# Performance work log

Measured on AMD Instinct MI355X. Metric: run time of the kernel, lower is better.

## Reference

```python
import jax, jax.numpy as jnp
import numpy as np

B, N, C, F, P, S = 128, 32, 1024, 14, 3, 2  # batch, boxes/img, channels, fmap size, pooled size, sampling ratio
NUM_BEHAVIORS = 27


def _interp(coords, size):
    # torchvision-style bilinear weights along one axis. coords: [M]
    valid = (coords > -1.0) & (coords < size)
    c = jnp.clip(coords, 0.0, size - 1.0)
    lo = jnp.clip(jnp.floor(c).astype(jnp.int32), 0, size - 2)
    hi = lo + 1
    f = c - lo.astype(c.dtype)
    wlo = jnp.where(valid, 1.0 - f, 0.0)
    whi = jnp.where(valid, f, 0.0)
    return lo, hi, wlo, whi


def _roi_one(fm, box):
    # fm: [C,H,W], box: [4] = (x1,y1,x2,y2) in fmap coords. Returns [C,P,P].
    x1, y1, x2, y2 = box[0], box[1], box[2], box[3]
    roi_w = jnp.maximum(x2 - x1, 1.0)
    roi_h = jnp.maximum(y2 - y1, 1.0)
    bh, bw = roi_h / P, roi_w / P
    offs = (jnp.arange(S, dtype=fm.dtype) + 0.5) / S  # sample offsets within a bin
    bins = jnp.arange(P, dtype=fm.dtype)
    ys = (y1 + bins[:, None] * bh + offs[None, :] * bh).reshape(-1)  # [P*S]
    xs = (x1 + bins[:, None] * bw + offs[None, :] * bw).reshape(-1)  # [P*S]
    ylo, yhi, wylo, wyhi = _interp(ys, F)
    xlo, xhi, wxlo, wxhi = _interp(xs, F)
    # separable bilinear gather: first along H, then along W
    fy = fm[:, ylo, :] * wylo[None, :, None] + fm[:, yhi, :] * wyhi[None, :, None]  # [C,M,W]
    v = fy[:, :, xlo] * wxlo[None, None, :] + fy[:, :, xhi] * wxhi[None, None, :]    # [C,M,M]
    return v.reshape(C, P, S, P, S).mean(axis=(2, 4))


def setup_inputs() -> dict:
    key = jax.random.key(0)
    ks = jax.random.split(key, 9)
    fmap = jax.random.normal(ks[0], (B, C, F, F), dtype=jnp.float32)
    # two random corner candidates per axis -> sorted gives valid (x1,y1,x2,y2) in [0,F]
    raw = jax.random.uniform(ks[1], (B, N, 2, 2), dtype=jnp.float32) * F
    lo = raw.min(axis=2)  # [B,N,2] -> (x1,y1)
    hi = raw.max(axis=2)  # [B,N,2] -> (x2,y2)
    boxes = jnp.concatenate([lo, hi], axis=-1)  # [B,N,4]
    w_c1 = jax.random.normal(ks[2], (512, 1024), dtype=jnp.float32) * 0.03
    w_c2 = jax.random.normal(ks[3], (256, 512), dtype=jnp.float32) * 0.04
    w_fc1 = jax.random.normal(ks[4], (2304, 1024), dtype=jnp.float32) * 0.02
    b_fc1 = jax.random.normal(ks[5], (1024,), dtype=jnp.float32) * 0.01
    w_fc2 = jax.random.normal(ks[6], (1024, NUM_BEHAVIORS), dtype=jnp.float32) * 0.03
    b_fc2 = jax.random.normal(ks[7], (NUM_BEHAVIORS,), dtype=jnp.float32) * 0.01
    return {"fmap": fmap, "boxes": boxes, "w_c1": w_c1, "w_c2": w_c2,
            "w_fc1": w_fc1, "b_fc1": b_fc1, "w_fc2": w_fc2, "b_fc2": b_fc2}


def reference(fmap, boxes, w_c1, w_c2, w_fc1, b_fc1, w_fc2, b_fc2):
    boxes = jnp.clip(boxes, 0.0, float(F))  # torch.clamp(box, 0, fmap_size)
    # per-image, per-box ROIAlign without duplicating fmap per box
    pooled = jax.vmap(lambda fm, bxs: jax.vmap(lambda b: _roi_one(fm, b))(bxs))(fmap, boxes)
    pooled = jax.lax.stop_gradient(pooled)  # fmap.detach() + no_grad roi_align
    x = pooled.reshape(B * N, C, P, P)
    x = jnp.einsum('kchw,oc->kohw', x, w_c1)  # 1x1 conv, no bias
    x = jnp.einsum('kchw,oc->kohw', x, w_c2)  # 1x1 conv, no bias
    x = x.reshape(B * N, -1)                  # [K, 256*3*3] (C,H,W order as in torch .view)
    h = jax.nn.relu(x @ w_fc1 + b_fc1)        # dropout inactive (eval / deterministic ref)
    logits = h @ w_fc2 + b_fc2                # [K, num_behaviors]
    return logits
```

## Files before the change

kernel.cpp:

```cpp
#include <hip/hip_runtime.h>

typedef unsigned short ushortT;
typedef __attribute__((ext_vector_type(8))) short short8;
typedef __attribute__((ext_vector_type(4))) short short4v;
typedef __attribute__((ext_vector_type(8))) __bf16 bf16x8;
typedef __attribute__((ext_vector_type(4))) float f32x4;

__device__ __forceinline__ float bf2f(ushortT u) {
    unsigned int x = ((unsigned int)u) << 16;
    return __builtin_bit_cast(float, x);
}
__device__ __forceinline__ ushortT f2bf(float f) {
    unsigned int x = __builtin_bit_cast(unsigned int, f);
    unsigned int r = (x + 0x7FFFu + ((x >> 16) & 1u)) >> 16;
    return (ushortT)r;
}

__device__ __forceinline__ void gload_lds16(const void* g, void* l) {
    __builtin_amdgcn_global_load_lds(
        (const __attribute__((address_space(1))) void*)g,
        (__attribute__((address_space(3))) void*)l, 16, 0, 0);
}

__global__ __launch_bounds__(256)
void build_wct_part(const float* __restrict__ w_c1, const float* __restrict__ w_c2,
                    float* __restrict__ part)
{
    __shared__ float w2s[64][65];
    __shared__ float w1s[64][65];
    const int o0 = blockIdx.x * 64;
    const int c0 = blockIdx.y * 64;
    const int m0 = blockIdx.z * 128;
    const int tid = threadIdx.x;
    const int ty = tid >> 4, tx = tid & 15;
    float acc[4][4] = {};
    for (int mm = 0; mm < 128; mm += 64) {
        #pragma unroll
        for (int c4 = 0; c4 < 4; ++c4) {
            int idx = c4 * 256 + tid;
            int row = idx >> 4, f4 = idx & 15;
            float4 v = *reinterpret_cast<const float4*>(
                w_c2 + (size_t)(o0 + row) * 512 + m0 + mm + f4 * 4);
            w2s[row][f4*4+0] = v.x; w2s[row][f4*4+1] = v.y;
            w2s[row][f4*4+2] = v.z; w2s[row][f4*4+3] = v.w;
            float4 u = *reinterpret_cast<const float4*>(
                w_c1 + (size_t)(m0 + mm + row) * 1024 + c0 + f4 * 4);
            w1s[row][f4*4+0] = u.x; w1s[row][f4*4+1] = u.y;
            w1s[row][f4*4+2] = u.z; w1s[row][f4*4+3] = u.w;
        }
        __syncthreads();
        for (int m = 0; m < 64; ++m) {
            float a[4], b[4];
            #pragma unroll
            for (int i = 0; i < 4; ++i) a[i] = w2s[ty*4+i][m];
            #pragma unroll
            for (int j = 0; j < 4; ++j) b[j] = w1s[m][tx*4+j];
            #pragma unroll
            for (int i = 0; i < 4; ++i)
                #pragma unroll
                for (int j = 0; j < 4; ++j) acc[i][j] = fmaf(a[i], b[j], acc[i][j]);
        }
        __syncthreads();
    }
    float* dst = part + (size_t)blockIdx.z * 262144;
    #pragma unroll
    for (int i = 0; i < 4; ++i) {
        float4 ov = { acc[i][0], acc[i][1], acc[i][2], acc[i][3] };
        *reinterpret_cast<float4*>(dst + (size_t)(o0 + ty*4 + i) * 1024 + c0 + tx*4) = ov;
    }
}

__global__ __launch_bounds__(256)
void wct_reduce(const float* __restrict__ part, ushortT* __restrict__ Wct_t)
{
    const int i = blockIdx.x * 256 + threadIdx.x;
    float4 s0 = *reinterpret_cast<const float4*>(part + (size_t)i * 4);
    float4 s1 = *reinterpret_cast<const float4*>(part + 262144 + (size_t)i * 4);
    float4 s2 = *reinterpret_cast<const float4*>(part + 524288 + (size_t)i * 4);
    float4 s3 = *reinterpret_cast<const float4*>(part + 786432 + (size_t)i * 4);
    short4v ov = { (short)f2bf(s0.x + s1.x + s2.x + s3.x),
                   (short)f2bf(s0.y + s1.y + s2.y + s3.y),
                   (short)f2bf(s0.z + s1.z + s2.z + s3.z),
                   (short)f2bf(s0.w + s1.w + s2.w + s3.w) };
    *reinterpret_cast<short4v*>(Wct_t + (size_t)i * 4) = ov;
}

__global__ __launch_bounds__(256)
void permute_fc1(const float* __restrict__ w_fc1, ushortT* __restrict__ wpt)
{
    __shared__ float tile[64][65];
    const int ci0 = blockIdx.x * 64;
    const int j0  = blockIdx.y * 64;
    const int hw  = ci0 >> 8;
    const int o0  = ci0 & 255;
    const int tid = threadIdx.x;
    #pragma unroll
    for (int c4 = 0; c4 < 4; ++c4) {
        int idx = c4 * 256 + tid;
        int row = idx >> 4;
        int f4  = idx & 15;
        float4 v = *reinterpret_cast<const float4*>(
            w_fc1 + (size_t)((o0 + row) * 9 + hw) * 1024 + j0 + f4 * 4);
        tile[row][f4*4+0] = v.x; tile[row][f4*4+1] = v.y;
        tile[row][f4*4+2] = v.z; tile[row][f4*4+3] = v.w;
    }
    __syncthreads();
    #pragma unroll
    for (int c4 = 0; c4 < 4; ++c4) {
        int idx = c4 * 256 + tid;
        int j   = idx >> 4;
        int og  = idx & 15;
        short4v ov;
        #pragma unroll
        for (int i = 0; i < 4; ++i) ov[i] = (short)f2bf(tile[og*4+i][j]);
        *reinterpret_cast<short4v*>(wpt + (size_t)(j0 + j) * 2304 + ci0 + og*4) = ov;
    }
}

__global__ __launch_bounds__(256)
void transpose_bf(const float* __restrict__ fmap, ushortT* __restrict__ fT)
{
    __shared__ ushortT tile[196][72];
    const int b   = blockIdx.x >> 4;
    const int c0  = (blockIdx.x & 15) << 6;
    const int tid = threadIdx.x;

    #pragma unroll
    for (int it = 0; it < 4; ++it) {
        int item = it * 256 + tid;
        if (item < 784) {
            int c4g = item / 49;
            int q   = item - c4g * 49;
            const float* s = fmap + ((size_t)b * 1024 + c0 + c4g * 4) * 196 + q * 4;
            float4 v0 = *reinterpret_cast<const float4*>(s);
            float4 v1 = *reinterpret_cast<const float4*>(s + 196);
            float4 v2 = *reinterpret_cast<const float4*>(s + 392);
            float4 v3 = *reinterpret_cast<const float4*>(s + 588);
            int p = q * 4, cc = c4g * 4;
            short4v w0 = {(short)f2bf(v0.x),(short)f2bf(v1.x),(short)f2bf(v2.x),(short)f2bf(v3.x)};
            short4v w1 = {(short)f2bf(v0.y),(short)f2bf(v1.y),(short)f2bf(v2.y),(short)f2bf(v3.y)};
            short4v w2 = {(short)f2bf(v0.z),(short)f2bf(v1.z),(short)f2bf(v2.z),(short)f2bf(v3.z)};
            short4v w3 = {(short)f2bf(v0.w),(short)f2bf(v1.w),(short)f2bf(v2.w),(short)f2bf(v3.w)};
            *reinterpret_cast<short4v*>(&tile[p+0][cc]) = w0;
            *reinterpret_cast<short4v*>(&tile[p+1][cc]) = w1;
            *reinterpret_cast<short4v*>(&tile[p+2][cc]) = w2;
            *reinterpret_cast<short4v*>(&tile[p+3][cc]) = w3;
        }
    }
    __syncthreads();

    #pragma unroll
    for (int it = 0; it < 7; ++it) {
        int item = it * 256 + tid;
        if (item < 1568) {
            int p  = item >> 3;
            int c8 = (item & 7) * 8;
            short8 v = *reinterpret_cast<const short8*>(&tile[p][c8]);
            *reinterpret_cast<short8*>(fT + ((size_t)b * 196 + p) * 1024 + c0 + c8) = v;
        }
    }
}

__global__ __launch_bounds__(256)
void roi_lite(const ushortT* __restrict__ fmap2, const float* __restrict__ boxes,
              ushortT* __restrict__ pooled)
{
    __shared__ ushortT tile[196][72];
    const int b   = blockIdx.x >> 2;
    const int o0  = (blockIdx.x & 3) << 6;
    const int tid = threadIdx.x;

    const ushortT* src = fmap2 + (size_t)b * 196 * 256 + o0;
    #pragma unroll
    for (int i = 0; i < 7; ++i) {
        int chunk = tid + (i << 8);
        if (chunk < 1568) {
            int p  = chunk >> 3;
            int c8 = (chunk & 7) << 3;
            short8 v = *reinterpret_cast<const short8*>(src + (size_t)p * 256 + c8);
            *reinterpret_cast<short8*>(&tile[p][c8]) = v;
        }
    }
    __syncthreads();

    const int box = tid >> 3;
    const int ch8 = (tid & 7) << 3;
    const int k   = (b << 5) + box;
    const float* bx = boxes + (size_t)k * 4;
    float x1 = fminf(fmaxf(bx[0], 0.f), 14.f);
    float y1 = fminf(fmaxf(bx[1], 0.f), 14.f);
    float x2 = fminf(fmaxf(bx[2], 0.f), 14.f);
    float y2 = fminf(fmaxf(bx[3], 0.f), 14.f);
    float bw = fmaxf(x2 - x1, 1.f) * (1.0f / 3.0f);
    float bh = fmaxf(y2 - y1, 1.f) * (1.0f / 3.0f);

    int   ylo[6], xlo[6];
    float wylo[6], wyhi[6], wxlo[6], wxhi[6];
    #pragma unroll
    for (int i = 0; i < 6; ++i) {
        float off = (i & 1) ? 0.75f : 0.25f;
        float pf  = (float)(i >> 1);
        float yc = y1 + (pf + off) * bh;
        bool  vy = (yc > -1.0f) && (yc < 14.f);
        float cy = fminf(fmaxf(yc, 0.f), 13.f);
        int   lo = (int)floorf(cy); if (lo > 12) lo = 12;
        float fy = cy - (float)lo;
        ylo[i]  = lo;
        wylo[i] = vy ? 1.f - fy : 0.f;
        wyhi[i] = vy ? fy       : 0.f;
        float xc = x1 + (pf + off) * bw;
        bool  vx = (xc > -1.0f) && (xc < 14.f);
        float cx = fminf(fmaxf(xc, 0.f), 13.f);
        int   lx = (int)floorf(cx); if (lx > 12) lx = 12;
        float fx = cx - (float)lx;
        xlo[i]  = lx;
        wxlo[i] = vx ? 1.f - fx : 0.f;
        wxhi[i] = vx ? fx       : 0.f;
    }

    float acc[3][3][8] = {};
    #pragma unroll
    for (int i = 0; i < 6; ++i) {
        #pragma unroll
        for (int j = 0; j < 6; ++j) {
            const int plo = ylo[i] * 14 + xlo[j];
            const float w00 = wylo[i] * wxlo[j];
            const float w01 = wylo[i] * wxhi[j];
            const float w10 = wyhi[i] * wxlo[j];
            const float w11 = wyhi[i] * wxhi[j];
            short8 v00 = *reinterpret_cast<const short8*>(&tile[plo][ch8]);
            short8 v01 = *reinterpret_cast<const short8*>(&tile[plo + 1][ch8]);
            short8 v10 = *reinterpret_cast<const short8*>(&tile[plo + 14][ch8]);
            short8 v11 = *reinterpret_cast<const short8*>(&tile[plo + 15][ch8]);
            #pragma unroll
            for (int c = 0; c < 8; ++c) {
                float a = acc[i >> 1][j >> 1][c];
                a = fmaf(bf2f((ushortT)v00[c]), w00, a);
                a = fmaf(bf2f((ushortT)v01[c]), w01, a);
                a = fmaf(bf2f((ushortT)v10[c]), w10, a);
                a = fmaf(bf2f((ushortT)v11[c]), w11, a);
                acc[i >> 1][j >> 1][c] = a;
            }
        }
    }

    ushortT* outp = pooled + (size_t)k * 2304 + o0 + ch8;
    #pragma unroll
    for (int p = 0; p < 3; ++p) {
        #pragma unroll
        for (int q = 0; q < 3; ++q) {
            short8 ov;
            #pragma unroll
            for (int c = 0; c < 8; ++c) ov[c] = (short)f2bf(acc[p][q][c] * 0.25f);
            *reinterpret_cast<short8*>(outp + (size_t)(p * 3 + q) * 256) = ov;
        }
    }
}

template<int RELU, int BIAS>
__global__ __launch_bounds__(256, 2)
void gemm_mfma(const ushortT* __restrict__ A, const ushortT* __restrict__ Bt,
               ushortT* __restrict__ C, const float* __restrict__ bias,
               int M, int N, int K)
{
    __shared__ ushortT As[2][128 * 64];
    const int tid  = threadIdx.x;
    const int wid  = tid >> 6;
    const int lane = tid & 63;
    const int ncolb = N >> 6;
    const int nblk  = (M >> 7) * ncolb;
    const int cpx   = nblk >> 3;
    const int i     = blockIdx.x;
    const int w     = (i & 7) * cpx + (i >> 3);
    const size_t row0 = (size_t)(w / ncolb) * 128;
    const size_t col0 = (size_t)(w % ncolb) * 64;

    const ushortT* agbase = A + row0 * K;
    auto stage = [&](int k0, int buf) {
        #pragma unroll
        for (int q = 0; q < 4; ++q) {
            int id  = q * 256 + tid;
            int row = id >> 3;
            int kcs = (id & 7) ^ (row & 7);
            gload_lds16(agbase + (size_t)row * K + k0 + kcs * 8,
                        As[buf] + id * 8);
        }
    };

    const int fr = lane & 15;
    const int kq = lane >> 4;
    const int rx = fr & 7;
    auto lda = [&](const ushortT* Ab, int m, int s) -> bf16x8 {
        const int r = m * 16 + fr;
        const int c = (s << 2) + kq;
        return *reinterpret_cast<const bf16x8*>(&Ab[(r << 6) + ((c ^ rx) << 3)]);
    };

    const ushortT* bbase = Bt + (col0 + wid * 16 + fr) * (size_t)K + kq * 8;
    auto loadB2 = [&](int k0, bf16x8& r0, bf16x8& r1) {
        r0 = *reinterpret_cast<const bf16x8*>(bbase + k0);
        r1 = *reinterpret_cast<const bf16x8*>(bbase + k0 + 32);
    };

    f32x4 acc[8];
    #pragma unroll
    for (int m = 0; m < 8; ++m) acc[m] = (f32x4){0,0,0,0};

    auto domfma = [&](const ushortT* Ab, bf16x8 b0, bf16x8 b1) {
        #pragma unroll
        for (int m = 0; m < 8; ++m) {
            acc[m] = __builtin_amdgcn_mfma_f32_16x16x32_bf16(lda(Ab, m, 0), b0, acc[m], 0, 0, 0);
            acc[m] = __builtin_amdgcn_mfma_f32_16x16x32_bf16(lda(Ab, m, 1), b1, acc[m], 0, 0, 0);
        }
    };

    const int nsteps = K >> 6;
    bf16x8 bA0, bA1, bB0, bB1;
    stage(0, 0);
    loadB2(0, bA0, bA1);
    __syncthreads();

    #pragma unroll 1
    for (int s = 0; s < (nsteps >> 1); ++s) {
        const int t = 2 * s;
        if (t + 1 < nsteps) { stage((t + 1) * 64, 1); loadB2((t + 1) * 64, bB0, bB1); }
        domfma(As[0], bA0, bA1);
        __syncthreads();
        if (t + 2 < nsteps) { stage((t + 2) * 64, 0); loadB2((t + 2) * 64, bA0, bA1); }
        domfma(As[1], bB0, bB1);
        __syncthreads();
    }

    const int orow = kq * 4;
    const size_t col = col0 + wid * 16 + fr;
    float bv = 0.f;
    if (BIAS) bv = bias[col];
    #pragma unroll
    for (int m = 0; m < 8; ++m) {
        const size_t rbase = row0 + m * 16 + orow;
        #pragma unroll
        for (int j = 0; j < 4; ++j) {
            float v = acc[m][j] + bv;
            if (RELU) v = fmaxf(v, 0.f);
            C[(rbase + j) * N + col] = f2bf(v);
        }
    }
}

__global__ __launch_bounds__(256)
void fc2_kernel(const ushortT* __restrict__ h, const float* __restrict__ w,
                const float* __restrict__ bias, float* __restrict__ out)
{
    __shared__ float   Wsm[128][32];
    __shared__ ushortT Hs[16][136];
    const int tid  = threadIdx.x;
    const int row0 = blockIdx.x * 16;
    const int r    = tid >> 4;
    const int jg   = tid & 15;
    float accx = 0.f, accy = 0.f;

    const int kk2  = tid >> 1;
    const int half = tid & 1;

    for (int k0 = 0; k0 < 1024; k0 += 128) {
        if (half == 0) {
            #pragma unroll
            for (int j = 0; j < 14; ++j)
                Wsm[kk2][j] = w[(size_t)(k0 + kk2) * 27 + j];
        } else {
            #pragma unroll
            for (int j = 14; j < 27; ++j)
                Wsm[kk2][j] = w[(size_t)(k0 + kk2) * 27 + j];
            #pragma unroll
            for (int j = 27; j < 32; ++j) Wsm[kk2][j] = 0.f;
        }
        {
            int hr = tid >> 4, hc = tid & 15;
            short8 v = *reinterpret_cast<const short8*>(
                h + (size_t)(row0 + hr) * 1024 + k0 + hc * 8);
            *reinterpret_cast<short8*>(&Hs[hr][hc * 8]) = v;
        }
        __syncthreads();
        #pragma unroll 8
        for (int kk = 0; kk < 128; ++kk) {
            float  hv = bf2f(Hs[r][kk]);
            float2 wv = *reinterpret_cast<const float2*>(&Wsm[kk][jg * 2]);
            accx = fmaf(hv, wv.x, accx);
            accy = fmaf(hv, wv.y, accy);
        }
        __syncthreads();
    }
    const int j0 = jg * 2;
    float* op = out + (size_t)(row0 + r) * 27;
    if (j0 < 27)     op[j0]     = accx + bias[j0];
    if (j0 + 1 < 27) op[j0 + 1] = accy + bias[j0 + 1];
}

extern "C" void kernel_launch(void* const* d_in, const int* in_sizes, int n_in,
                              void* d_out, int out_size, void* d_ws, size_t ws_size,
                              hipStream_t stream)
{
    (void)in_sizes; (void)n_in; (void)out_size; (void)ws_size;
    const float* fmap  = (const float*)d_in[0];
    const float* boxes = (const float*)d_in[1];
    const float* w_c1  = (const float*)d_in[2];
    const float* w_c2  = (const float*)d_in[3];
    const float* w_fc1 = (const float*)d_in[4];
    const float* b_fc1 = (const float*)d_in[5];
    const float* w_fc2 = (const float*)d_in[6];
    const float* b_fc2 = (const float*)d_in[7];
    float* out = (float*)d_out;

    char* ws = (char*)d_ws;
    size_t off = 0;
    ushortT* fmapT  = (ushortT*)(ws + off); off += (size_t)25088 * 1024 * 2;
    ushortT* fmap2  = (ushortT*)(ws + off); off += (size_t)25088 * 256 * 2;
    ushortT* pooled = (ushortT*)(ws + off); off += (size_t)4096 * 2304 * 2;
    ushortT* hbuf   = (ushortT*)(ws + off); off += (size_t)4096 * 1024 * 2;
    ushortT* Wct_t  = (ushortT*)(ws + off); off += (size_t)256 * 1024 * 2;
    ushortT* wp_t   = (ushortT*)(ws + off); off += (size_t)1024 * 2304 * 2;
    float*   wpart  = (float*)(ws + off);   off += (size_t)4 * 262144 * 4;

    hipLaunchKernelGGL(build_wct_part, dim3(4, 16, 4), dim3(256), 0, stream, w_c1, w_c2, wpart);
    hipLaunchKernelGGL(wct_reduce,     dim3(256),      dim3(256), 0, stream, wpart, Wct_t);
    hipLaunchKernelGGL(permute_fc1,    dim3(36, 16),   dim3(256), 0, stream, w_fc1, wp_t);
    hipLaunchKernelGGL(transpose_bf,   dim3(2048),     dim3(256), 0, stream, fmap, fmapT);

    hipLaunchKernelGGL((gemm_mfma<0,0>), dim3(784), dim3(256), 0, stream,
                       fmapT, Wct_t, fmap2, (const float*)nullptr, 25088, 256, 1024);
    hipLaunchKernelGGL(roi_lite, dim3(512), dim3(256), 0, stream, fmap2, boxes, pooled);
    hipLaunchKernelGGL((gemm_mfma<1,1>), dim3(512), dim3(256), 0, stream,
                       pooled, wp_t, hbuf, b_fc1, 4096, 1024, 2304);
    hipLaunchKernelGGL(fc2_kernel, dim3(256), dim3(256), 0, stream,
                       hbuf, w_fc2, b_fc2, out);
}
```

Before: 150.3 us.

## Fuse preprocessing kernels into one launch and drop split-K weight product

Merges the fmap transpose/bf16 cast, the w_c2·w_c1 weight product, and the fc1 weight permute into a single kernel that dispatches on block index. The combined-conv weight product no longer uses a four-way split-K with a separate reduction kernel. Each of its 64 blocks now loops over the full K of 512 and writes bf16 directly. This removes three launches and the fp32 partial buffer round trip. In exchange the 64 weight-product blocks each run four times longer and may become a straggler tail in the fused grid.

```diff
diff --git a/kernel.cpp b/kernel.cpp
--- a/kernel.cpp
+++ b/kernel.cpp
@@ -23,140 +23,125 @@
 }
 
 __global__ __launch_bounds__(256)
-void build_wct_part(const float* __restrict__ w_c1, const float* __restrict__ w_c2,
-                    float* __restrict__ part)
+void prep_fused(const float* __restrict__ fmap,
+                const float* __restrict__ w_c1, const float* __restrict__ w_c2,
+                const float* __restrict__ w_fc1,
+                ushortT* __restrict__ fT, ushortT* __restrict__ Wct_t,
+                ushortT* __restrict__ wpt)
 {
-    __shared__ float w2s[64][65];
-    __shared__ float w1s[64][65];
-    const int o0 = blockIdx.x * 64;
-    const int c0 = blockIdx.y * 64;
-    const int m0 = blockIdx.z * 128;
+    __shared__ __align__(16) char smem[33280];
+    const int blk = blockIdx.x;
     const int tid = threadIdx.x;
-    const int ty = tid >> 4, tx = tid & 15;
-    float acc[4][4] = {};
-    for (int mm = 0; mm < 128; mm += 64) {
+
+    if (blk < 2048) {
+        auto tile = reinterpret_cast<ushortT(*)[72]>(smem);
+        const int b  = blk >> 4;
+        const int c0 = (blk & 15) << 6;
+
+        #pragma unroll
+        for (int it = 0; it < 4; ++it) {
+            int item = it * 256 + tid;
+            if (item < 784) {
+                int c4g = item / 49;
+                int q   = item - c4g * 49;
+                const float* s = fmap + ((size_t)b * 1024 + c0 + c4g * 4) * 196 + q * 4;
+                float4 v0 = *reinterpret_cast<const float4*>(s);
+                float4 v1 = *reinterpret_cast<const float4*>(s + 196);
+                float4 v2 = *reinterpret_cast<const float4*>(s + 392);
+                float4 v3 = *reinterpret_cast<const float4*>(s + 588);
+                int p = q * 4, cc = c4g * 4;
+                short4v w0 = {(short)f2bf(v0.x),(short)f2bf(v1.x),(short)f2bf(v2.x),(short)f2bf(v3.x)};
+                short4v w1 = {(short)f2bf(v0.y),(short)f2bf(v1.y),(short)f2bf(v2.y),(short)f2bf(v3.y)};
+                short4v w2 = {(short)f2bf(v0.z),(short)f2bf(v1.z),(short)f2bf(v2.z),(short)f2bf(v3.z)};
+                short4v w3 = {(short)f2bf(v0.w),(short)f2bf(v1.w),(short)f2bf(v2.w),(short)f2bf(v3.w)};
+                *reinterpret_cast<short4v*>(&tile[p+0][cc]) = w0;
+                *reinterpret_cast<short4v*>(&tile[p+1][cc]) = w1;
+                *reinterpret_cast<short4v*>(&tile[p+2][cc]) = w2;
+                *reinterpret_cast<short4v*>(&tile[p+3][cc]) = w3;
+            }
+        }
+        __syncthreads();
+        #pragma unroll
+        for (int it = 0; it < 7; ++it) {
+            int item = it * 256 + tid;
+            if (item < 1568) {
+                int p  = item >> 3;
+                int c8 = (item & 7) * 8;
+                short8 v = *reinterpret_cast<const short8*>(&tile[p][c8]);
+                *reinterpret_cast<short8*>(fT + ((size_t)b * 196 + p) * 1024 + c0 + c8) = v;
+            }
+        }
+    } else if (blk < 2112) {
+        auto w2s = reinterpret_cast<float(*)[65]>(smem);
+        auto w1s = reinterpret_cast<float(*)[65]>(smem + 16640);
+        const int idx = blk - 2048;
+        const int o0 = (idx & 3) * 64;
+        const int c0 = (idx >> 2) * 64;
+        const int ty = tid >> 4, tx = tid & 15;
+        float acc[4][4] = {};
+        for (int m0 = 0; m0 < 512; m0 += 64) {
+            #pragma unroll
+            for (int c4 = 0; c4 < 4; ++c4) {
+                int id2 = c4 * 256 + tid;
+                int row = id2 >> 4, f4 = id2 & 15;
+                float4 v = *reinterpret_cast<const float4*>(
+                    w_c2 + (size_t)(o0 + row) * 512 + m0 + f4 * 4);
+                w2s[row][f4*4+0] = v.x; w2s[row][f4*4+1] = v.y;
+                w2s[row][f4*4+2] = v.z; w2s[row][f4*4+3] = v.w;
+                float4 u = *reinterpret_cast<const float4*>(
+                    w_c1 + (size_t)(m0 + row) * 1024 + c0 + f4 * 4);
+                w1s[row][f4*4+0] = u.x; w1s[row][f4*4+1] = u.y;
+                w1s[row][f4*4+2] = u.z; w1s[row][f4*4+3] = u.w;
+            }
+            __syncthreads();
+            for (int m = 0; m < 64; ++m) {
+                float a[4], b[4];
+                #pragma unroll
+                for (int i = 0; i < 4; ++i) a[i] = w2s[ty*4+i][m];
+                #pragma unroll
+                for (int j = 0; j < 4; ++j) b[j] = w1s[m][tx*4+j];
+                #pragma unroll
+                for (int i = 0; i < 4; ++i)
+                    #pragma unroll
+                    for (int j = 0; j < 4; ++j) acc[i][j] = fmaf(a[i], b[j], acc[i][j]);
+            }
+            __syncthreads();
+        }
+        #pragma unroll
+        for (int i = 0; i < 4; ++i) {
+            short4v ov;
+            #pragma unroll
+            for (int j = 0; j < 4; ++j) ov[j] = (short)f2bf(acc[i][j]);
+            *reinterpret_cast<short4v*>(Wct_t + (size_t)(o0 + ty*4 + i) * 1024 + c0 + tx*4) = ov;
+        }
+    } else {
+        auto tile = reinterpret_cast<float(*)[65]>(smem);
+        const int idx = blk - 2112;
+        const int cib = idx % 36;
+        const int ci0 = cib * 64;
+        const int j0  = (idx / 36) * 64;
+        const int hw  = ci0 >> 8;
+        const int o0  = ci0 & 255;
         #pragma unroll
         for (int c4 = 0; c4 < 4; ++c4) {
-            int idx = c4 * 256 + tid;
-            int row = idx >> 4, f4 = idx & 15;
+            int id2 = c4 * 256 + tid;
+            int row = id2 >> 4;
+            int f4  = id2 & 15;
             float4 v = *reinterpret_cast<const float4*>(
-                w_c2 + (size_t)(o0 + row) * 512 + m0 + mm + f4 * 4);
-            w2s[row][f4*4+0] = v.x; w2s[row][f4*4+1] = v.y;
-            w2s[row][f4*4+2] = v.z; w2s[row][f4*4+3] = v.w;
-            float4 u = *reinterpret_cast<const float4*>(
-                w_c1 + (size_t)(m0 + mm + row) * 1024 + c0 + f4 * 4);
-            w1s[row][f4*4+0] = u.x; w1s[row][f4*4+1] = u.y;
-            w1s[row][f4*4+2] = u.z; w1s[row][f4*4+3] = u.w;
-        }
-        __syncthreads();
-        for (int m = 0; m < 64; ++m) {
-            float a[4], b[4];
-            #pragma unroll
-            for (int i = 0; i < 4; ++i) a[i] = w2s[ty*4+i][m];
-            #pragma unroll
-            for (int j = 0; j < 4; ++j) b[j] = w1s[m][tx*4+j];
-            #pragma unroll
-            for (int i = 0; i < 4; ++i)
-                #pragma unroll
-                for (int j = 0; j < 4; ++j) acc[i][j] = fmaf(a[i], b[j], acc[i][j]);
-        }
-        __syncthreads();
-    }
-    float* dst = part + (size_t)blockIdx.z * 262144;
-    #pragma unroll
-    for (int i = 0; i < 4; ++i) {
-        float4 ov = { acc[i][0], acc[i][1], acc[i][2], acc[i][3] };
-        *reinterpret_cast<float4*>(dst + (size_t)(o0 + ty*4 + i) * 1024 + c0 + tx*4) = ov;
-    }
-}
-
-__global__ __launch_bounds__(256)
-void wct_reduce(const float* __restrict__ part, ushortT* __restrict__ Wct_t)
-{
-    const int i = blockIdx.x * 256 + threadIdx.x;
-    float4 s0 = *reinterpret_cast<const float4*>(part + (size_t)i * 4);
-    float4 s1 = *reinterpret_cast<const float4*>(part + 262144 + (size_t)i * 4);
-    float4 s2 = *reinterpret_cast<const float4*>(part + 524288 + (size_t)i * 4);
-    float4 s3 = *reinterpret_cast<const float4*>(part + 786432 + (size_t)i * 4);
-    short4v ov = { (short)f2bf(s0.x + s1.x + s2.x + s3.x),
-                   (short)f2bf(s0.y + s1.y + s2.y + s3.y),
-                   (short)f2bf(s0.z + s1.z + s2.z + s3.z),
-                   (short)f2bf(s0.w + s1.w + s2.w + s3.w) };
-    *reinterpret_cast<short4v*>(Wct_t + (size_t)i * 4) = ov;
-}
-
-__global__ __launch_bounds__(256)
-void permute_fc1(const float* __restrict__ w_fc1, ushortT* __restrict__ wpt)
-{
-    __shared__ float tile[64][65];
-    const int ci0 = blockIdx.x * 64;
-    const int j0  = blockIdx.y * 64;
-    const int hw  = ci0 >> 8;
-    const int o0  = ci0 & 255;
-    const int tid = threadIdx.x;
-    #pragma unroll
-    for (int c4 = 0; c4 < 4; ++c4) {
-        int idx = c4 * 256 + tid;
-        int row = idx >> 4;
-        int f4  = idx & 15;
-        float4 v = *reinterpret_cast<const float4*>(
-            w_fc1 + (size_t)((o0 + row) * 9 + hw) * 1024 + j0 + f4 * 4);
-        tile[row][f4*4+0] = v.x; tile[row][f4*4+1] = v.y;
-        tile[row][f4*4+2] = v.z; tile[row][f4*4+3] = v.w;
-    }
-    __syncthreads();
-    #pragma unroll
-    for (int c4 = 0; c4 < 4; ++c4) {
-        int idx = c4 * 256 + tid;
-        int j   = idx >> 4;
-        int og  = idx & 15;
-        short4v ov;
-        #pragma unroll
-        for (int i = 0; i < 4; ++i) ov[i] = (short)f2bf(tile[og*4+i][j]);
-        *reinterpret_cast<short4v*>(wpt + (size_t)(j0 + j) * 2304 + ci0 + og*4) = ov;
-    }
-}
-
-__global__ __launch_bounds__(256)
-void transpose_bf(const float* __restrict__ fmap, ushortT* __restrict__ fT)
-{
-    __shared__ ushortT tile[196][72];
-    const int b   = blockIdx.x >> 4;
-    const int c0  = (blockIdx.x & 15) << 6;
-    const int tid = threadIdx.x;
-
-    #pragma unroll
-    for (int it = 0; it < 4; ++it) {
-        int item = it * 256 + tid;
-        if (item < 784) {
-            int c4g = item / 49;
-            int q   = item - c4g * 49;
-            const float* s = fmap + ((size_t)b * 1024 + c0 + c4g * 4) * 196 + q * 4;
-            float4 v0 = *reinterpret_cast<const float4*>(s);
-            float4 v1 = *reinterpret_cast<const float4*>(s + 196);
-            float4 v2 = *reinterpret_cast<const float4*>(s + 392);
-            float4 v3 = *reinterpret_cast<const float4*>(s + 588);
-            int p = q * 4, cc = c4g * 4;
-            short4v w0 = {(short)f2bf(v0.x),(short)f2bf(v1.x),(short)f2bf(v2.x),(short)f2bf(v3.x)};
-            short4v w1 = {(short)f2bf(v0.y),(short)f2bf(v1.y),(short)f2bf(v2.y),(short)f2bf(v3.y)};
-            short4v w2 = {(short)f2bf(v0.z),(short)f2bf(v1.z),(short)f2bf(v2.z),(short)f2bf(v3.z)};
-            short4v w3 = {(short)f2bf(v0.w),(short)f2bf(v1.w),(short)f2bf(v2.w),(short)f2bf(v3.w)};
-            *reinterpret_cast<short4v*>(&tile[p+0][cc]) = w0;
-            *reinterpret_cast<short4v*>(&tile[p+1][cc]) = w1;
-            *reinterpret_cast<short4v*>(&tile[p+2][cc]) = w2;
-            *reinterpret_cast<short4v*>(&tile[p+3][cc]) = w3;
-        }
-    }
-    __syncthreads();
-
-    #pragma unroll
-    for (int it = 0; it < 7; ++it) {
-        int item = it * 256 + tid;
-        if (item < 1568) {
-            int p  = item >> 3;
-            int c8 = (item & 7) * 8;
-            short8 v = *reinterpret_cast<const short8*>(&tile[p][c8]);
-            *reinterpret_cast<short8*>(fT + ((size_t)b * 196 + p) * 1024 + c0 + c8) = v;
+                w_fc1 + (size_t)((o0 + row) * 9 + hw) * 1024 + j0 + f4 * 4);
+            tile[row][f4*4+0] = v.x; tile[row][f4*4+1] = v.y;
+            tile[row][f4*4+2] = v.z; tile[row][f4*4+3] = v.w;
+        }
+        __syncthreads();
+        #pragma unroll
+        for (int c4 = 0; c4 < 4; ++c4) {
+            int id2 = c4 * 256 + tid;
+            int j   = id2 >> 4;
+            int og  = id2 & 15;
+            short4v ov;
+            #pragma unroll
+            for (int i = 0; i < 4; ++i) ov[i] = (short)f2bf(tile[og*4+i][j]);
+            *reinterpret_cast<short4v*>(wpt + (size_t)(j0 + j) * 2304 + ci0 + og*4) = ov;
         }
     }
 }
@@ -419,12 +404,9 @@
     ushortT* hbuf   = (ushortT*)(ws + off); off += (size_t)4096 * 1024 * 2;
     ushortT* Wct_t  = (ushortT*)(ws + off); off += (size_t)256 * 1024 * 2;
     ushortT* wp_t   = (ushortT*)(ws + off); off += (size_t)1024 * 2304 * 2;
-    float*   wpart  = (float*)(ws + off);   off += (size_t)4 * 262144 * 4;
-
-    hipLaunchKernelGGL(build_wct_part, dim3(4, 16, 4), dim3(256), 0, stream, w_c1, w_c2, wpart);
-    hipLaunchKernelGGL(wct_reduce,     dim3(256),      dim3(256), 0, stream, wpart, Wct_t);
-    hipLaunchKernelGGL(permute_fc1,    dim3(36, 16),   dim3(256), 0, stream, w_fc1, wp_t);
-    hipLaunchKernelGGL(transpose_bf,   dim3(2048),     dim3(256), 0, stream, fmap, fmapT);
+
+    hipLaunchKernelGGL(prep_fused, dim3(2688), dim3(256), 0, stream,
+                       fmap, w_c1, w_c2, w_fc1, fmapT, Wct_t, wp_t);
 
     hipLaunchKernelGGL((gemm_mfma<0,0>), dim3(784), dim3(256), 0, stream,
                        fmapT, Wct_t, fmap2, (const float*)nullptr, 25088, 256, 1024);
```

Result: slower. 177.4 us (+18.0%).
